# Kernel optimization log

Hardware: AMD Instinct MI355X
Metric: run time of the kernel (lower is better)

The kernel has to match this reference:

```python
import jax, jax.numpy as jnp
import numpy as np

D = 256
B, S, N = 4, 512, 4


def setup_inputs() -> dict:
    key = jax.random.key(0)
    ks = jax.random.split(key, 24)
    d, dq = D, D // 4
    std = 0.02
    inp = {
        'x':   jax.random.normal(ks[0], (B, S, N, d), jnp.float32),
        'Wq':  jax.random.normal(ks[1], (d, d), jnp.float32) * std,
        'Wk':  jax.random.normal(ks[2], (d, d), jnp.float32) * std,
        'Wv':  jax.random.normal(ks[3], (d, d), jnp.float32) * std,
        'Wg1': jax.random.normal(ks[4], (d, d), jnp.float32) * std,
        'bg1': jnp.zeros((d,), jnp.float32),
        'Wg2': jax.random.normal(ks[5], (d, d), jnp.float32) * std,
        'bg2': jnp.zeros((d,), jnp.float32),
        'We1': jax.random.normal(ks[6], (d, dq), jnp.float32) * std,
        'be1': jnp.zeros((dq,), jnp.float32),
        'We2': jax.random.normal(ks[7], (dq, 1), jnp.float32) * std,
        'be2': jnp.zeros((1,), jnp.float32),
        'Wa1': jax.random.normal(ks[8], (d, dq), jnp.float32) * std,
        'ba1': jnp.zeros((dq,), jnp.float32),
        'Wa2': jax.random.normal(ks[9], (dq, 1), jnp.float32) * std,
        'ba2': jnp.zeros((1,), jnp.float32),
        'Wo':  jax.random.normal(ks[10], (d, d), jnp.float32) * std,
        'bo':  jnp.zeros((d,), jnp.float32),
        'gamma': jnp.ones((d,), jnp.float32),
        'beta':  jnp.zeros((d,), jnp.float32),
    }
    return inp


def reference(x, Wq, Wk, Wv, Wg1, bg1, Wg2, bg2, We1, be1, We2, be2,
              Wa1, ba1, Wa2, ba2, Wo, bo, gamma, beta):
    b, s, n, f = x.shape
    xf = x.reshape(b * n, s, f)  # matches torch .view on contiguous x
    residual = xf

    q = xf @ Wq                                    # [bn, s, d]
    k = xf @ Wk
    v = xf @ Wv
    v_hat = jax.nn.silu(v @ Wg1 + bg1) @ Wg2 + bg2  # value_generator
    eta = jax.nn.sigmoid(jax.nn.silu(xf @ We1 + be1) @ We2 + be2) * 0.1 + 0.01   # [bn, s, 1]
    alpha = jax.nn.sigmoid(jax.nn.silu(xf @ Wa1 + ba1) @ Wa2 + ba2) * 0.5 + 0.5  # [bn, s, 1]

    # F.normalize(k, dim=-1): eps = 1e-12
    kn = k / jnp.maximum(jnp.linalg.norm(k, axis=-1, keepdims=True), 1e-12)

    M0 = jnp.zeros((b * n, f, f), x.dtype)

    def step(M, inp):
        q_t, k_t, v_t, e_t, a_t = inp  # [bn,d],[bn,d],[bn,d],[bn,1],[bn,1]
        out_t = jnp.einsum('bij,bj->bi', M, q_t)
        Mk = jnp.einsum('bij,bj->bi', M, k_t)
        e = e_t[:, :, None]  # [bn,1,1]
        a = a_t[:, :, None]
        # delta rule: M <- a*M - e*(Mk k^T) + e*(v k^T)
        M_new = a * M + e * ((v_t - Mk)[:, :, None] * k_t[:, None, :])
        return M_new, out_t

    seq = (jnp.swapaxes(q, 0, 1), jnp.swapaxes(kn, 0, 1), jnp.swapaxes(v_hat, 0, 1),
           jnp.swapaxes(eta, 0, 1), jnp.swapaxes(alpha, 0, 1))
    M, outs = jax.lax.scan(step, M0, seq)
    out = jnp.swapaxes(outs, 0, 1)  # [bn, s, d]

    y = out @ Wo + bo + residual  # dropout is identity in eval/reference
    mu = jnp.mean(y, axis=-1, keepdims=True)
    var = jnp.var(y, axis=-1, keepdims=True)
    y = (y - mu) / jnp.sqrt(var + 1e-5) * gamma + beta
    return y.reshape(b, s, n, f), M
```

## Files before the change

kernel.cpp:

```cpp
#include <hip/hip_runtime.h>

#define F_ 256
#define S_ 512
#define NH_ 16
#define CCH 32
#define NCH (S_/CCH)
#define KSTR 264
#define KTSTR 36
#define TSTR 40
#define PSTR 17

typedef __attribute__((ext_vector_type(8))) short short8_t;
typedef __attribute__((ext_vector_type(4))) float f32x4;

__device__ __forceinline__ float sigmoid_f(float x) { return 1.0f / (1.0f + __expf(-x)); }

__device__ __forceinline__ ushort f2bf(float x) {
  uint u = __float_as_uint(x);
  u += 0x7FFFu + ((u >> 16) & 1u);
  return (ushort)(u >> 16);
}
__device__ __forceinline__ float bf2f(ushort u) {
  return __uint_as_float((uint)u << 16);
}

template<int CTRL>
__device__ __forceinline__ float dpp_add(float x) {
  int y = __builtin_amdgcn_update_dpp(0, __float_as_int(x), CTRL, 0xf, 0xf, true);
  return x + __int_as_float(y);
}
__device__ __forceinline__ float red8(float x) {
  x = dpp_add<0xB1>(x);
  x = dpp_add<0x4E>(x);
  x = dpp_add<0x141>(x);
  return x;
}

__global__ __launch_bounds__(256) void wconv_k(
    const float* __restrict__ Wq, const float* __restrict__ Wk,
    const float* __restrict__ Wv, const float* __restrict__ Wg1,
    const float* __restrict__ Wg2, const float* __restrict__ Wo,
    const float* __restrict__ We1, const float* __restrict__ Wa1,
    const float* __restrict__ be1, const float* __restrict__ ba1,
    const float* __restrict__ x,
    ushort* __restrict__ Wt, float* __restrict__ beas,
    ushort* __restrict__ xb)
{
  const int blk = blockIdx.x, tid = threadIdx.x;
  if (blk >= 105) {
    const size_t base = (size_t)(blk - 105) * 16384;
    #pragma unroll
    for (int p = 0; p < 16; ++p) {
      const size_t o = base + (size_t)(((p << 8) + tid) << 2);
      const float4 v = *(const float4*)&x[o];
      ushort4 h4;
      h4.x = f2bf(v.x); h4.y = f2bf(v.y); h4.z = f2bf(v.z); h4.w = f2bf(v.w);
      *(ushort4*)&xb[o] = h4;
    }
    return;
  }
  if (blk == 104) {
    if (tid < 64) beas[tid] = be1[tid];
    else if (tid < 128) beas[tid] = ba1[tid - 64];
    return;
  }
  __shared__ float tile[64][65];
  const float* src; int N, k0, n0; size_t dstbase;
  if (blk < 96) {
    const int w = blk >> 4, tl = blk & 15;
    const float* ws_[6] = {Wq, Wk, Wv, Wg1, Wg2, Wo};
    const size_t dstb[6] = {0, 65536, 131072, 229376, 294912, 360448};
    src = ws_[w]; N = 256;
    k0 = (tl >> 2) * 64; n0 = (tl & 3) * 64;
    dstbase = dstb[w];
  } else {
    const int w = (blk - 96) >> 2, tl = (blk - 96) & 3;
    src = w ? Wa1 : We1; N = 64;
    k0 = tl * 64; n0 = 0;
    dstbase = w ? 212992 : 196608;
  }
  #pragma unroll
  for (int p = 0; p < 4; ++p) {
    const int idx = (p << 8) + tid;
    const int r = idx >> 4, c4 = (idx & 15) << 2;
    if (c4 < N) {
      const float4 v = *(const float4*)&src[(size_t)(k0 + r) * N + n0 + c4];
      tile[r][c4 + 0] = v.x; tile[r][c4 + 1] = v.y;
      tile[r][c4 + 2] = v.z; tile[r][c4 + 3] = v.w;
    }
  }
  __syncthreads();
  #pragma unroll
  for (int p = 0; p < 4; ++p) {
    const int idx = (p << 8) + tid;
    const int nl = idx >> 4, kc = (idx & 15) << 2;
    if (nl < ((blk < 96) ? 64 : 64) && (n0 + nl) < ((blk < 96) ? 256 : 64)) {
      ushort4 o;
      o.x = f2bf(tile[kc + 0][nl]); o.y = f2bf(tile[kc + 1][nl]);
      o.z = f2bf(tile[kc + 2][nl]); o.w = f2bf(tile[kc + 3][nl]);
      *(ushort4*)&Wt[dstbase + (size_t)(n0 + nl) * 256 + k0 + kc] = o;
    }
  }
}

__global__ __launch_bounds__(256) void qkve_k(
    const ushort* __restrict__ A, const ushort* __restrict__ Wt,
    const float* __restrict__ beas,
    ushort* __restrict__ qb, float* __restrict__ kf,
    ushort* __restrict__ vb, float* __restrict__ sesa)
{
  __shared__ ushort As[2][64 * 72];
  __shared__ ushort Ws[2][64 * 72];
  const int tid = threadIdx.x;
  const int wv = tid >> 6, l = tid & 63;
  const int ln = l & 15, hi = l >> 4, hi4 = hi << 2, hi8 = hi << 3;
  const int wr = wv >> 1, wc = wv & 1;
  const int row0 = blockIdx.y * 64, col0 = blockIdx.x * 64;
  const int r_ = tid >> 3, c8_ = (tid & 7) << 3;

  short8_t pA[2], pB[2];
  auto loadT = [&](int k0) {
    pA[0] = *(const short8_t*)&A[(size_t)(row0 + r_) * 256 + k0 + c8_];
    pA[1] = *(const short8_t*)&A[(size_t)(row0 + 32 + r_) * 256 + k0 + c8_];
    pB[0] = *(const short8_t*)&Wt[(size_t)(col0 + r_) * 256 + k0 + c8_];
    pB[1] = *(const short8_t*)&Wt[(size_t)(col0 + 32 + r_) * 256 + k0 + c8_];
  };
  auto commitT = [&](int b) {
    *(short8_t*)&As[b][r_ * 72 + c8_] = pA[0];
    *(short8_t*)&As[b][(32 + r_) * 72 + c8_] = pA[1];
    *(short8_t*)&Ws[b][r_ * 72 + c8_] = pB[0];
    *(short8_t*)&Ws[b][(32 + r_) * 72 + c8_] = pB[1];
  };

  f32x4 acc[2][2];
  #pragma unroll
  for (int i = 0; i < 2; ++i)
    #pragma unroll
    for (int j = 0; j < 2; ++j)
      #pragma unroll
      for (int r = 0; r < 4; ++r) acc[i][j][r] = 0.f;

  loadT(0); commitT(0); __syncthreads();
  #pragma unroll
  for (int t = 0; t < 4; ++t) {
    const int b = t & 1;
    if (t < 3) loadT((t + 1) << 6);
    #pragma unroll
    for (int kk = 0; kk < 2; ++kk) {
      short8_t a0 = *(const short8_t*)&As[b][(wr * 32 + ln) * 72 + kk * 32 + hi8];
      short8_t a1 = *(const short8_t*)&As[b][(wr * 32 + 16 + ln) * 72 + kk * 32 + hi8];
      short8_t b0 = *(const short8_t*)&Ws[b][(wc * 32 + ln) * 72 + kk * 32 + hi8];
      short8_t b1 = *(const short8_t*)&Ws[b][(wc * 32 + 16 + ln) * 72 + kk * 32 + hi8];
      acc[0][0] = __builtin_amdgcn_mfma_f32_16x16x32_bf16(a0, b0, acc[0][0], 0, 0, 0);
      acc[0][1] = __builtin_amdgcn_mfma_f32_16x16x32_bf16(a0, b1, acc[0][1], 0, 0, 0);
      acc[1][0] = __builtin_amdgcn_mfma_f32_16x16x32_bf16(a1, b0, acc[1][0], 0, 0, 0);
      acc[1][1] = __builtin_amdgcn_mfma_f32_16x16x32_bf16(a1, b1, acc[1][1], 0, 0, 0);
    }
    if (t < 3) commitT(b ^ 1);
    __syncthreads();
  }

  #pragma unroll
  for (int mi = 0; mi < 2; ++mi)
    #pragma unroll
    for (int ni = 0; ni < 2; ++ni) {
      const int col = col0 + wc * 32 + ni * 16 + ln;
      #pragma unroll
      for (int r = 0; r < 4; ++r) {
        const int row = row0 + wr * 32 + mi * 16 + hi4 + r;
        float vx = acc[mi][ni][r];
        if (col0 < 256)      qb[(size_t)row * 256 + col] = f2bf(vx);
        else if (col0 < 512) kf[(size_t)row * 256 + (col - 256)] = vx;
        else if (col0 < 768) vb[(size_t)row * 256 + (col - 512)] = f2bf(vx);
        else {
          const int cc = col - 768;
          vx += beas[cc];
          vx *= sigmoid_f(vx);
          sesa[(size_t)row * 128 + cc] = vx;
        }
      }
    }
}

__global__ __launch_bounds__(256) void gemm_bf16_k(
    const ushort* __restrict__ A, const ushort* __restrict__ Wt,
    const float* __restrict__ bias, float* __restrict__ Cf,
    ushort* __restrict__ Cb, int act)
{
  __shared__ ushort As[2][64 * 72];
  __shared__ ushort Ws[2][64 * 72];
  const int tid = threadIdx.x;
  const int wv = tid >> 6, l = tid & 63;
  const int ln = l & 15, hi = l >> 4, hi4 = hi << 2, hi8 = hi << 3;
  const int wr = wv >> 1, wc = wv & 1;
  const int row0 = blockIdx.y * 64, col0 = blockIdx.x * 64;
  const int r_ = tid >> 3, c8_ = (tid & 7) << 3;

  short8_t pA[2], pB[2];
  auto loadT = [&](int k0) {
    pA[0] = *(const short8_t*)&A[(size_t)(row0 + r_) * 256 + k0 + c8_];
    pA[1] = *(const short8_t*)&A[(size_t)(row0 + 32 + r_) * 256 + k0 + c8_];
    pB[0] = *(const short8_t*)&Wt[(size_t)(col0 + r_) * 256 + k0 + c8_];
    pB[1] = *(const short8_t*)&Wt[(size_t)(col0 + 32 + r_) * 256 + k0 + c8_];
  };
  auto commitT = [&](int b) {
    *(short8_t*)&As[b][r_ * 72 + c8_] = pA[0];
    *(short8_t*)&As[b][(32 + r_) * 72 + c8_] = pA[1];
    *(short8_t*)&Ws[b][r_ * 72 + c8_] = pB[0];
    *(short8_t*)&Ws[b][(32 + r_) * 72 + c8_] = pB[1];
  };

  f32x4 acc[2][2];
  #pragma unroll
  for (int i = 0; i < 2; ++i)
    #pragma unroll
    for (int j = 0; j < 2; ++j)
      #pragma unroll
      for (int r = 0; r < 4; ++r) acc[i][j][r] = 0.f;

  loadT(0); commitT(0); __syncthreads();
  #pragma unroll
  for (int t = 0; t < 4; ++t) {
    const int b = t & 1;
    if (t < 3) loadT((t + 1) << 6);
    #pragma unroll
    for (int kk = 0; kk < 2; ++kk) {
      short8_t a0 = *(const short8_t*)&As[b][(wr * 32 + ln) * 72 + kk * 32 + hi8];
      short8_t a1 = *(const short8_t*)&As[b][(wr * 32 + 16 + ln) * 72 + kk * 32 + hi8];
      short8_t b0 = *(const short8_t*)&Ws[b][(wc * 32 + ln) * 72 + kk * 32 + hi8];
      short8_t b1 = *(const short8_t*)&Ws[b][(wc * 32 + 16 + ln) * 72 + kk * 32 + hi8];
      acc[0][0] = __builtin_amdgcn_mfma_f32_16x16x32_bf16(a0, b0, acc[0][0], 0, 0, 0);
      acc[0][1] = __builtin_amdgcn_mfma_f32_16x16x32_bf16(a0, b1, acc[0][1], 0, 0, 0);
      acc[1][0] = __builtin_amdgcn_mfma_f32_16x16x32_bf16(a1, b0, acc[1][0], 0, 0, 0);
      acc[1][1] = __builtin_amdgcn_mfma_f32_16x16x32_bf16(a1, b1, acc[1][1], 0, 0, 0);
    }
    if (t < 3) commitT(b ^ 1);
    __syncthreads();
  }

  #pragma unroll
  for (int mi = 0; mi < 2; ++mi)
    #pragma unroll
    for (int ni = 0; ni < 2; ++ni) {
      const int col = col0 + wc * 32 + ni * 16 + ln;
      const float bval = bias ? bias[col] : 0.f;
      #pragma unroll
      for (int r = 0; r < 4; ++r) {
        const int row = row0 + wr * 32 + mi * 16 + hi4 + r;
        float vx = acc[mi][ni][r] + bval;
        if (act == 1) vx = vx * sigmoid_f(vx);
        if (Cf) Cf[(size_t)row * 256 + col] = vx;
        if (Cb) Cb[(size_t)row * 256 + col] = f2bf(vx);
      }
    }
}

__global__ __launch_bounds__(256) void knea_k(
    const float* __restrict__ kf, ushort* __restrict__ kb,
    const float* __restrict__ sesa,
    const float* __restrict__ We2, const float* __restrict__ be2,
    const float* __restrict__ Wa2, const float* __restrict__ ba2,
    float* __restrict__ eta, float* __restrict__ alpha)
{
  const int lane = threadIdx.x & 63;
  const size_t row = ((size_t)blockIdx.x << 2) + (threadIdx.x >> 6);
  {
    const size_t off = row * F_ + ((size_t)lane << 2);
    float4 v = *(const float4*)&kf[off];
    float ss = v.x * v.x + v.y * v.y + v.z * v.z + v.w * v.w;
    #pragma unroll
    for (int m = 1; m < 64; m <<= 1) ss += __shfl_xor(ss, m, 64);
    const float sc = 1.0f / fmaxf(sqrtf(ss), 1e-12f);
    ushort4 o;
    o.x = f2bf(v.x * sc); o.y = f2bf(v.y * sc);
    o.z = f2bf(v.z * sc); o.w = f2bf(v.w * sc);
    *(ushort4*)&kb[off] = o;
  }
  {
    float pe = sesa[row * 128 + lane] * We2[lane];
    float pa = sesa[row * 128 + 64 + lane] * Wa2[lane];
    #pragma unroll
    for (int m = 1; m < 64; m <<= 1) {
      pe += __shfl_xor(pe, m, 64);
      pa += __shfl_xor(pa, m, 64);
    }
    if (lane == 0) {
      eta[row]   = sigmoid_f(pe + be2[0]) * 0.1f + 0.01f;
      alpha[row] = sigmoid_f(pa + ba2[0]) * 0.5f + 0.5f;
    }
  }
}

__global__ __launch_bounds__(256) void ln_k(
    const float* __restrict__ t, const float* __restrict__ x,
    const float* __restrict__ gamma, const float* __restrict__ beta,
    float* __restrict__ y)
{
  const int lane = threadIdx.x & 63;
  const size_t row = ((size_t)blockIdx.x << 2) + (threadIdx.x >> 6);
  const size_t off = row * F_ + ((size_t)lane << 2);
  const float4 tv = *(const float4*)&t[off];
  const float4 xv = *(const float4*)&x[off];
  float4 v = make_float4(tv.x + xv.x, tv.y + xv.y, tv.z + xv.z, tv.w + xv.w);
  float sm = v.x + v.y + v.z + v.w;
  float sq = v.x * v.x + v.y * v.y + v.z * v.z + v.w * v.w;
  #pragma unroll
  for (int m = 1; m < 64; m <<= 1) {
    sm += __shfl_xor(sm, m, 64);
    sq += __shfl_xor(sq, m, 64);
  }
  const float mu  = sm * (1.0f / 256.0f);
  const float var = sq * (1.0f / 256.0f) - mu * mu;
  const float rstd = rsqrtf(var + 1e-5f);
  const float4 g = *(const float4*)&gamma[(size_t)lane << 2];
  const float4 b = *(const float4*)&beta[(size_t)lane << 2];
  float4 o;
  o.x = (v.x - mu) * rstd * g.x + b.x;
  o.y = (v.y - mu) * rstd * g.y + b.y;
  o.z = (v.z - mu) * rstd * g.z + b.z;
  o.w = (v.w - mu) * rstd * g.w + b.w;
  *(float4*)&y[off] = o;
}

__global__ __launch_bounds__(256) void prep_k(
    const ushort* __restrict__ kb, const ushort* __restrict__ qb,
    const float* __restrict__ eta, const float* __restrict__ alpha,
    ushort* __restrict__ Tg, ushort* __restrict__ Gqg, float* __restrict__ Sg,
    ushort* __restrict__ Ktg)
{
  __shared__ ushort K_lds[CCH * KSTR];
  __shared__ ushort Q_lds[CCH * KSTR];
  __shared__ float  G_lds[CCH * CCH];
  __shared__ float  ea[2 * CCH];
  __shared__ float  scal[100];

  const int tid = threadIdx.x;
  const int ch = blockIdx.x, h = blockIdx.y;
  const int t0 = ch * CCH;
  const int l = tid & 63, wv = tid >> 6;
  const int ln = l & 15, hi = l >> 4;
  const int hi8 = hi * 8, hi4 = hi * 4;

  const ushort* kg = kb + (size_t)(h * S_ + t0) * F_;
  const ushort* qg = qb + (size_t)(h * S_ + t0) * F_;
  #pragma unroll
  for (int w = 0; w < 4; ++w) {
    int o = w * 256 + tid; int t = o >> 5, c8 = (o & 31) << 3;
    *(short8_t*)&K_lds[t * KSTR + c8] = *(const short8_t*)&kg[(size_t)t * F_ + c8];
    *(short8_t*)&Q_lds[t * KSTR + c8] = *(const short8_t*)&qg[(size_t)t * F_ + c8];
  }
  if (tid < CCH)            ea[tid] = eta[(size_t)h * S_ + t0 + tid];
  else if (tid < 2 * CCH)   ea[tid] = alpha[(size_t)h * S_ + t0 + tid - CCH];
  __syncthreads();

  {
    const int tt = tid & 31, cl = tid >> 5;
    for (int cp = 0; cp < 32; ++cp) {
      const int c = cp * 8 + cl;
      Ktg[((size_t)h * F_ + c) * S_ + t0 + tt] = K_lds[tt * KSTR + c];
    }
  }

  {
    const int tI = wv >> 1, tJ = wv & 1;
    f32x4 accG = {0.f, 0.f, 0.f, 0.f};
    f32x4 accQ = {0.f, 0.f, 0.f, 0.f};
    #pragma unroll
    for (int ko = 0; ko < 8; ++ko) {
      const int cb = ko * 32 + hi8;
      short8_t bfr = *(const short8_t*)&K_lds[(tJ * 16 + ln) * KSTR + cb];
      short8_t aK  = *(const short8_t*)&K_lds[(tI * 16 + ln) * KSTR + cb];
      short8_t aQ  = *(const short8_t*)&Q_lds[(tI * 16 + ln) * KSTR + cb];
      accG = __builtin_amdgcn_mfma_f32_16x16x32_bf16(aK, bfr, accG, 0, 0, 0);
      accQ = __builtin_amdgcn_mfma_f32_16x16x32_bf16(aQ, bfr, accQ, 0, 0, 0);
    }
    ushort* Gqo = Gqg + (size_t)(h * NCH + ch) * (CCH * CCH);
    #pragma unroll
    for (int r = 0; r < 4; ++r) {
      const int t = tI * 16 + hi4 + r, s = tJ * 16 + ln;
      G_lds[t * CCH + s] = accG[r];
      Gqo[t * CCH + s] = (s < t) ? f2bf(accQ[r]) : (ushort)0;
    }
  }
  if (tid == 0) {
    float gp = 1.f;
    for (int t = 0; t < CCH; ++t) {
      const float a = ea[CCH + t], e = ea[t];
      const float gm = gp * a;
      scal[t]           = e / a;
      scal[CCH + t]     = e / gm;
      scal[2 * CCH + t] = gp;
      gp = gm;
    }
    scal[3 * CCH] = gp;
  }
  __syncthreads();

  {
    const int j = tid >> 3, g = tid & 7;
    float x0 = 0.f, x1 = 0.f, x2 = 0.f, x3 = 0.f;
    ushort* To = Tg + (size_t)(h * NCH + ch) * (CCH * CCH);
    #pragma unroll
    for (int t = 0; t < CCH; ++t) {
      float p = 0.f;
      const f32x4 gr = *(const f32x4*)&G_lds[t * CCH + 4 * g];
      if (4 * g + 0 < t) p += gr[0] * x0;
      if (4 * g + 1 < t) p += gr[1] * x1;
      if (4 * g + 2 < t) p += gr[2] * x2;
      if (4 * g + 3 < t) p += gr[3] * x3;
      const float tot = red8(p);
      const float xt = ((t == j) ? 1.f : 0.f) - scal[t] * tot;
      if (g == (t >> 2)) {
        if ((t & 3) == 0) x0 = xt; else if ((t & 3) == 1) x1 = xt;
        else if ((t & 3) == 2) x2 = xt; else x3 = xt;
      }
      if (g == 0) To[t * CCH + j] = f2bf(xt);
    }
  }
  if (tid < 97) Sg[(size_t)(h * NCH + ch) * 128 + tid] = scal[tid];
}

__global__ __launch_bounds__(256, 1) void scan_chunk_k(
    const ushort* __restrict__ kb, const ushort* __restrict__ qb,
    const ushort* __restrict__ vhb, const ushort* __restrict__ Ktg,
    const ushort* __restrict__ Tg, const ushort* __restrict__ Gqg,
    const float* __restrict__ Sg,
    ushort* __restrict__ outb, float* __restrict__ Mout)
{
  __shared__ ushort K_lds[CCH * KSTR];
  __shared__ ushort Q_lds[CCH * KSTR];
  __shared__ ushort Kt_lds[2][F_ * KTSTR];
  __shared__ ushort M_lds[2][16 * KSTR];
  __shared__ ushort T_lds[CCH * TSTR];
  __shared__ ushort Gq_lds[2][CCH * TSTR];
  __shared__ ushort Wt_lds[16 * TSTR];
  __shared__ ushort R_lds[16 * TSTR];
  __shared__ float  KMp[4 * CCH * PSTR];
  __shared__ float  QM_lds[CCH * PSTR];
  __shared__ ushort V_lds[CCH * 16];
  __shared__ float  scal[2][104];

  const int tid = threadIdx.x;
  const int flat = blockIdx.x;
  const int h = (flat & 7) + ((flat >> 7) << 3);
  const int slice = (flat >> 3) & 15;
  const int r0 = slice * 16;
  const int wv = tid >> 6, l = tid & 63;
  const int ln = l & 15, hi = l >> 4, hi4 = hi << 2, hi8 = hi << 3;

  for (int u = tid; u < 16 * KSTR / 8; u += 256) {
    short8_t z = {0, 0, 0, 0, 0, 0, 0, 0};
    *(short8_t*)&M_lds[0][u * 8] = z;
  }
  f32x4 Mf[4];
  #pragma unroll
  for (int q = 0; q < 4; ++q)
    #pragma unroll
    for (int r = 0; r < 4; ++r) Mf[q][r] = 0.f;

  const ushort* kgh = kb + (size_t)h * S_ * F_;
  const ushort* qgh = qb + (size_t)h * S_ * F_;
  const ushort* kth = Ktg + (size_t)h * F_ * S_;

  short8_t pK[4], pQ[4], pKt[4], pTG;
  ushort pV[2]; float pS = 0.f;

  auto loadchunk = [&](int ch) {
    const int t0 = ch * CCH;
    #pragma unroll
    for (int r = 0; r < 4; ++r) {
      const int idx = (r << 8) + tid;
      const int t = idx >> 5, c8 = (idx & 31) << 3;
      pK[r] = *(const short8_t*)&kgh[(size_t)(t0 + t) * F_ + c8];
      pQ[r] = *(const short8_t*)&qgh[(size_t)(t0 + t) * F_ + c8];
    }
    #pragma unroll
    for (int r = 0; r < 4; ++r) {
      const int idx = (r << 8) + tid;
      const int c = idx >> 2, t8 = (idx & 3) << 3;
      pKt[r] = *(const short8_t*)&kth[(size_t)c * S_ + t0 + t8];
    }
    #pragma unroll
    for (int u = 0; u < 2; ++u) {
      const int e = (u << 8) + tid, t = e >> 4, i = e & 15;
      pV[u] = vhb[(size_t)(h * S_ + t0 + t) * F_ + r0 + i];
    }
    {
      const ushort* Ti = Tg  + (size_t)(h * NCH + ch) * (CCH * CCH);
      const ushort* Gi = Gqg + (size_t)(h * NCH + ch) * (CCH * CCH);
      if (tid < 128) {
        const int t = tid >> 2, c8 = (tid & 3) << 3;
        pTG = *(const short8_t*)&Ti[t * CCH + c8];
      } else {
        const int t = (tid - 128) >> 2, c8 = ((tid - 128) & 3) << 3;
        pTG = *(const short8_t*)&Gi[t * CCH + c8];
      }
    }
    if (tid < 97) pS = Sg[(size_t)(h * NCH + ch) * 128 + tid];
  };

  auto commit = [&](int b) {
    #pragma unroll
    for (int r = 0; r < 4; ++r) {
      const int idx = (r << 8) + tid;
      const int t = idx >> 5, c8 = (idx & 31) << 3;
      *(short8_t*)&K_lds[t * KSTR + c8] = pK[r];
      *(short8_t*)&Q_lds[t * KSTR + c8] = pQ[r];
    }
    #pragma unroll
    for (int r = 0; r < 4; ++r) {
      const int idx = (r << 8) + tid;
      const int c = idx >> 2, t8 = (idx & 3) << 3;
      *(short8_t*)&Kt_lds[b][c * KTSTR + t8] = pKt[r];
    }
    #pragma unroll
    for (int u = 0; u < 2; ++u) V_lds[(u << 8) + tid] = pV[u];
    if (tid < 128) {
      const int t = tid >> 2, c8 = (tid & 3) << 3;
      *(short8_t*)&T_lds[t * TSTR + c8] = pTG;
    } else {
      const int t = (tid - 128) >> 2, c8 = ((tid - 128) & 3) << 3;
      *(short8_t*)&Gq_lds[b][t * TSTR + c8] = pTG;
    }
    if (tid < 97) scal[b][tid] = pS;
  };

  loadchunk(0);
  commit(0);
  __syncthreads();
  int cb = 0;

  for (int ch = 0; ch < NCH; ++ch) {
    const int t0 = ch * CCH;
    const int nb = cb ^ 1;
    if (ch + 1 < NCH) loadchunk(ch + 1);

    {
      const int j0 = wv * 64;
      f32x4 a0v = {0.f, 0.f, 0.f, 0.f};
      f32x4 a1v = {0.f, 0.f, 0.f, 0.f};
      #pragma unroll
      for (int ks = 0; ks < 2; ++ks) {
        const int jc = j0 + ks * 32 + hi8;
        short8_t bm = *(const short8_t*)&M_lds[cb][ln * KSTR + jc];
        short8_t a0 = *(const short8_t*)&K_lds[ln * KSTR + jc];
        short8_t a1 = *(const short8_t*)&K_lds[(16 + ln) * KSTR + jc];
        a0v = __builtin_amdgcn_mfma_f32_16x16x32_bf16(a0, bm, a0v, 0, 0, 0);
        a1v = __builtin_amdgcn_mfma_f32_16x16x32_bf16(a1, bm, a1v, 0, 0, 0);
      }
      #pragma unroll
      for (int r = 0; r < 4; ++r) {
        KMp[wv * (CCH * PSTR) + (hi4 + r) * PSTR + ln] = a0v[r];
        KMp[wv * (CCH * PSTR) + (16 + hi4 + r) * PSTR + ln] = a1v[r];
      }
    }
    __syncthreads();

    if (wv == 0) {
      const int i = l & 15, tg = l >> 4;
      short8_t rv;
      #pragma unroll
      for (int u = 0; u < 8; ++u) {
        const int t = tg * 8 + u;
        const float s = KMp[t * PSTR + i]
                      + KMp[CCH * PSTR + t * PSTR + i]
                      + KMp[2 * CCH * PSTR + t * PSTR + i]
                      + KMp[3 * CCH * PSTR + t * PSTR + i];
        const float rhs = scal[cb][CCH + t] * bf2f(V_lds[t * 16 + i])
                        - scal[cb][t] * s;
        rv[u] = (short)f2bf(rhs);
      }
      *(short8_t*)&R_lds[i * TSTR + tg * 8] = rv;
      #pragma unroll
      for (int I = 0; I < 2; ++I) {
        short8_t a = *(const short8_t*)&T_lds[(I * 16 + ln) * TSTR + hi8];
        short8_t b = *(const short8_t*)&R_lds[ln * TSTR + hi8];
        f32x4 z = {0.f, 0.f, 0.f, 0.f};
        f32x4 d = __builtin_amdgcn_mfma_f32_16x16x32_bf16(a, b, z, 0, 0, 0);
        ushort4 wo;
        wo.x = f2bf(d[0]); wo.y = f2bf(d[1]); wo.z = f2bf(d[2]); wo.w = f2bf(d[3]);
        *(ushort4*)&Wt_lds[ln * TSTR + I * 16 + hi4] = wo;
      }
    } else if (wv >= 2) {
      const int I = wv - 2;
      f32x4 acc = {0.f, 0.f, 0.f, 0.f};
      #pragma unroll
      for (int ko = 0; ko < 8; ++ko) {
        short8_t a = *(const short8_t*)&Q_lds[(I * 16 + ln) * KSTR + ko * 32 + hi8];
        short8_t b = *(const short8_t*)&M_lds[cb][ln * KSTR + ko * 32 + hi8];
        acc = __builtin_amdgcn_mfma_f32_16x16x32_bf16(a, b, acc, 0, 0, 0);
      }
      #pragma unroll
      for (int r = 0; r < 4; ++r)
        QM_lds[(I * 16 + hi4 + r) * PSTR + ln] = acc[r];
    }
    __syncthreads();

    {
      const float gC = scal[cb][3 * CCH];
      short8_t aw = *(const short8_t*)&Wt_lds[ln * TSTR + hi8];
      #pragma unroll
      for (int qq = 0; qq < 4; ++qq) {
        const int jt = wv * 4 + qq;
        short8_t bk = *(const short8_t*)&Kt_lds[cb][(jt * 16 + ln) * KTSTR + hi8];
        f32x4 d = __builtin_amdgcn_mfma_f32_16x16x32_bf16(aw, bk, Mf[qq], 0, 0, 0);
        #pragma unroll
        for (int r = 0; r < 4; ++r) {
          const float nv = gC * d[r];
          Mf[qq][r] = nv;
          M_lds[nb][(hi4 + r) * KSTR + jt * 16 + ln] = f2bf(nv);
        }
      }
    }
    if (wv < 2) {
      const int I = wv;
      short8_t a = *(const short8_t*)&Gq_lds[cb][(I * 16 + ln) * TSTR + hi8];
      short8_t b = *(const short8_t*)&Wt_lds[ln * TSTR + hi8];
      f32x4 z = {0.f, 0.f, 0.f, 0.f};
      f32x4 d = __builtin_amdgcn_mfma_f32_16x16x32_bf16(a, b, z, 0, 0, 0);
      #pragma unroll
      for (int r = 0; r < 4; ++r) {
        const int t = I * 16 + hi4 + r;
        const float ov = scal[cb][2 * CCH + t] * (QM_lds[t * PSTR + ln] + d[r]);
        outb[(size_t)(h * S_ + t0 + t) * F_ + r0 + ln] = f2bf(ov);
      }
    }
    if (ch + 1 < NCH) commit(nb);
    __syncthreads();
    cb = nb;
  }

  #pragma unroll
  for (int qq = 0; qq < 4; ++qq) {
    const int jt = wv * 4 + qq;
    #pragma unroll
    for (int r = 0; r < 4; ++r)
      Mout[((size_t)h * F_ + r0 + hi4 + r) * F_ + jt * 16 + ln] = Mf[qq][r];
  }
}

extern "C" void kernel_launch(void* const* d_in, const int* in_sizes, int n_in,
                              void* d_out, int out_size, void* d_ws, size_t ws_size,
                              hipStream_t stream)
{
  const float* x    = (const float*)d_in[0];
  const float* Wq   = (const float*)d_in[1];
  const float* Wk   = (const float*)d_in[2];
  const float* Wv   = (const float*)d_in[3];
  const float* Wg1  = (const float*)d_in[4];
  const float* bg1  = (const float*)d_in[5];
  const float* Wg2  = (const float*)d_in[6];
  const float* bg2  = (const float*)d_in[7];
  const float* We1  = (const float*)d_in[8];
  const float* be1  = (const float*)d_in[9];
  const float* We2  = (const float*)d_in[10];
  const float* be2  = (const float*)d_in[11];
  const float* Wa1  = (const float*)d_in[12];
  const float* ba1  = (const float*)d_in[13];
  const float* Wa2  = (const float*)d_in[14];
  const float* ba2  = (const float*)d_in[15];
  const float* Wo   = (const float*)d_in[16];
  const float* bo   = (const float*)d_in[17];
  const float* gamma= (const float*)d_in[18];
  const float* beta = (const float*)d_in[19];

  const int Mrows = NH_ * S_;
  const size_t MM = 1048576;
  const size_t NTF = 2 * MM;

  float* ws = (float*)d_ws;
  ushort* xb   = (ushort*)(ws + 0 * MM);
  ushort* outb = (ushort*)(ws + 0 * MM);
  ushort* qb   = (ushort*)(ws + 1 * MM);
  ushort* kb   = (ushort*)(ws + 2 * MM);
  float*  kf   = ws + 3 * MM;
  ushort* t1b  = (ushort*)(ws + 3 * MM);
  ushort* vhb  = (ushort*)(ws + 4 * MM);
  ushort* vb   = (ushort*)(ws + 5 * MM);
  float*  sesa = ws + 6 * MM;
  float*  ytmp = ws + 5 * MM;
  float*  eta  = ws + 7 * MM;
  float*  alpha= eta + Mrows;
  ushort* Tg   = (ushort*)(ws + 7 * MM + 16384);
  ushort* Gqg  = Tg + 262144;
  float*  Sg   = ws + 7 * MM + 16384 + 131072 + 131072;
  ushort* Ktg  = (ushort*)(Sg + 32768);
  ushort* Wt   = Ktg + 2097152;
  float*  beas = (float*)(Wt + 425984);

  dim3 blk(256);

  wconv_k<<<233, blk, 0, stream>>>(Wq, Wk, Wv, Wg1, Wg2, Wo, We1, Wa1,
                                   be1, ba1, x, Wt, beas, xb);

  qkve_k<<<dim3(14, 128), blk, 0, stream>>>(xb, Wt, beas, qb, kf, vb, sesa);

  knea_k<<<Mrows / 4, blk, 0, stream>>>(kf, kb, sesa, We2, be2, Wa2, ba2, eta, alpha);

  gemm_bf16_k<<<dim3(4, 128), blk, 0, stream>>>(vb,  Wt + 229376, bg1, nullptr, t1b, 1);
  gemm_bf16_k<<<dim3(4, 128), blk, 0, stream>>>(t1b, Wt + 294912, bg2, nullptr, vhb, 0);

  prep_k<<<dim3(NCH, NH_), blk, 0, stream>>>(kb, qb, eta, alpha, Tg, Gqg, Sg, Ktg);

  float* yout = (float*)d_out;
  float* Mfin = yout + NTF;
  scan_chunk_k<<<256, blk, 0, stream>>>(kb, qb, vhb, Ktg, Tg, Gqg, Sg, outb, Mfin);

  gemm_bf16_k<<<dim3(4, 128), blk, 0, stream>>>(outb, Wt + 360448, bo, ytmp, nullptr, 0);
  ln_k<<<Mrows / 4, blk, 0, stream>>>(ytmp, x, gamma, beta, yout);
}
```

Baseline: 101.2 us.

## Restructure chunked scan: two row-slices per 512-thread block, MFMA operands from registers

The chunked delta-rule scan kernel now runs 512-thread blocks, each handling two 16-row slices of the state matrix. K, Q, K-transpose and the T/Gq operands are loaded straight into registers in MFMA fragment layout, so the LDS staging buffers, the commit pass and most LDS traffic go away. Work is also reassigned across waves: K·M and Q·M are split over four waves, which halves the KMp reduction. In exchange, each block is larger, only 128 blocks are launched, register pressure rises, and global loads for K-transpose now sit on the critical path within each chunk.

```diff
diff --git a/kernel.cpp b/kernel.cpp
--- a/kernel.cpp
+++ b/kernel.cpp
@@ -6,9 +6,7 @@
 #define CCH 32
 #define NCH (S_/CCH)
 #define KSTR 264
-#define KTSTR 36
 #define TSTR 40
-#define PSTR 17
 
 typedef __attribute__((ext_vector_type(8))) short short8_t;
 typedef __attribute__((ext_vector_type(4))) float f32x4;
@@ -94,7 +92,7 @@
   for (int p = 0; p < 4; ++p) {
     const int idx = (p << 8) + tid;
     const int nl = idx >> 4, kc = (idx & 15) << 2;
-    if (nl < ((blk < 96) ? 64 : 64) && (n0 + nl) < ((blk < 96) ? 256 : 64)) {
+    if ((n0 + nl) < ((blk < 96) ? 256 : 64)) {
       ushort4 o;
       o.x = f2bf(tile[kc + 0][nl]); o.y = f2bf(tile[kc + 1][nl]);
       o.z = f2bf(tile[kc + 2][nl]); o.w = f2bf(tile[kc + 3][nl]);
@@ -420,36 +418,40 @@
   if (tid < 97) Sg[(size_t)(h * NCH + ch) * 128 + tid] = scal[tid];
 }
 
-__global__ __launch_bounds__(256, 1) void scan_chunk_k(
+__global__ __launch_bounds__(512, 1) void scan_chunk_k(
     const ushort* __restrict__ kb, const ushort* __restrict__ qb,
     const ushort* __restrict__ vhb, const ushort* __restrict__ Ktg,
     const ushort* __restrict__ Tg, const ushort* __restrict__ Gqg,
     const float* __restrict__ Sg,
     ushort* __restrict__ outb, float* __restrict__ Mout)
 {
-  __shared__ ushort K_lds[CCH * KSTR];
-  __shared__ ushort Q_lds[CCH * KSTR];
-  __shared__ ushort Kt_lds[2][F_ * KTSTR];
   __shared__ ushort M_lds[2][16 * KSTR];
-  __shared__ ushort T_lds[CCH * TSTR];
-  __shared__ ushort Gq_lds[2][CCH * TSTR];
-  __shared__ ushort Wt_lds[16 * TSTR];
-  __shared__ ushort R_lds[16 * TSTR];
-  __shared__ float  KMp[4 * CCH * PSTR];
-  __shared__ float  QM_lds[CCH * PSTR];
-  __shared__ ushort V_lds[CCH * 16];
-  __shared__ float  scal[2][104];
+  __shared__ float  KMp[2][2 * CCH * 17];
+  __shared__ float  QM_lds[2][CCH * 17];
+  __shared__ ushort R_lds[2][16 * TSTR];
+  __shared__ ushort Wt_lds[2][16 * TSTR];
+  __shared__ ushort V_lds[2][CCH * 16];
+  __shared__ float  scal_lds[100];
 
   const int tid = threadIdx.x;
+  const int wave = tid >> 6;
+  const int cn = wave >> 2;
+  const int wv4 = wave & 3;
+  const int l = tid & 63;
+  const int ln = l & 15, hi = l >> 4, hi4 = hi << 2, hi8 = hi << 3;
   const int flat = blockIdx.x;
-  const int h = (flat & 7) + ((flat >> 7) << 3);
-  const int slice = (flat >> 3) & 15;
+  const int h = (flat & 7) + (((flat >> 3) & 1) << 3);
+  const int sp = flat >> 4;
+  const int slice = sp * 2 + cn;
   const int r0 = slice * 16;
-  const int wv = tid >> 6, l = tid & 63;
-  const int ln = l & 15, hi = l >> 4, hi4 = hi << 2, hi8 = hi << 3;
-
-  for (int u = tid; u < 16 * KSTR / 8; u += 256) {
-    short8_t z = {0, 0, 0, 0, 0, 0, 0, 0};
+
+  const ushort* kgh = kb  + (size_t)h * S_ * F_;
+  const ushort* qgh = qb  + (size_t)h * S_ * F_;
+  const ushort* kth = Ktg + (size_t)h * F_ * S_;
+  const ushort* vgh = vhb + (size_t)h * S_ * F_;
+
+  for (int u = tid; u < 2 * 16 * KSTR / 8; u += 512) {
+    short8_t z = {0,0,0,0,0,0,0,0};
     *(short8_t*)&M_lds[0][u * 8] = z;
   }
   f32x4 Mf[4];
@@ -458,181 +460,145 @@
     #pragma unroll
     for (int r = 0; r < 4; ++r) Mf[q][r] = 0.f;
 
-  const ushort* kgh = kb + (size_t)h * S_ * F_;
-  const ushort* qgh = qb + (size_t)h * S_ * F_;
-  const ushort* kth = Ktg + (size_t)h * F_ * S_;
-
-  short8_t pK[4], pQ[4], pKt[4], pTG;
-  ushort pV[2]; float pS = 0.f;
-
-  auto loadchunk = [&](int ch) {
+  short8_t pP1[8];
+  float pS = 0.f;
+  auto loadP1 = [&](int ch) {
     const int t0 = ch * CCH;
-    #pragma unroll
-    for (int r = 0; r < 4; ++r) {
-      const int idx = (r << 8) + tid;
-      const int t = idx >> 5, c8 = (idx & 31) << 3;
-      pK[r] = *(const short8_t*)&kgh[(size_t)(t0 + t) * F_ + c8];
-      pQ[r] = *(const short8_t*)&qgh[(size_t)(t0 + t) * F_ + c8];
-    }
-    #pragma unroll
-    for (int r = 0; r < 4; ++r) {
-      const int idx = (r << 8) + tid;
-      const int c = idx >> 2, t8 = (idx & 3) << 3;
-      pKt[r] = *(const short8_t*)&kth[(size_t)c * S_ + t0 + t8];
-    }
-    #pragma unroll
-    for (int u = 0; u < 2; ++u) {
-      const int e = (u << 8) + tid, t = e >> 4, i = e & 15;
-      pV[u] = vhb[(size_t)(h * S_ + t0 + t) * F_ + r0 + i];
-    }
-    {
-      const ushort* Ti = Tg  + (size_t)(h * NCH + ch) * (CCH * CCH);
-      const ushort* Gi = Gqg + (size_t)(h * NCH + ch) * (CCH * CCH);
-      if (tid < 128) {
-        const int t = tid >> 2, c8 = (tid & 3) << 3;
-        pTG = *(const short8_t*)&Ti[t * CCH + c8];
-      } else {
-        const int t = (tid - 128) >> 2, c8 = ((tid - 128) & 3) << 3;
-        pTG = *(const short8_t*)&Gi[t * CCH + c8];
-      }
-    }
+    if (wv4 < 2) {
+      #pragma unroll
+      for (int tt = 0; tt < 2; ++tt)
+        #pragma unroll
+        for (int ks = 0; ks < 4; ++ks)
+          pP1[tt * 4 + ks] = *(const short8_t*)
+            &kgh[(size_t)(t0 + tt * 16 + ln) * 256 + wv4 * 128 + ks * 32 + hi8];
+    } else {
+      const int t16 = (wv4 - 2) * 16;
+      #pragma unroll
+      for (int ko = 0; ko < 8; ++ko)
+        pP1[ko] = *(const short8_t*)
+          &qgh[(size_t)(t0 + t16 + ln) * 256 + ko * 32 + hi8];
+    }
+  };
+  auto loadS = [&](int ch) {
     if (tid < 97) pS = Sg[(size_t)(h * NCH + ch) * 128 + tid];
   };
 
-  auto commit = [&](int b) {
-    #pragma unroll
-    for (int r = 0; r < 4; ++r) {
-      const int idx = (r << 8) + tid;
-      const int t = idx >> 5, c8 = (idx & 31) << 3;
-      *(short8_t*)&K_lds[t * KSTR + c8] = pK[r];
-      *(short8_t*)&Q_lds[t * KSTR + c8] = pQ[r];
-    }
-    #pragma unroll
-    for (int r = 0; r < 4; ++r) {
-      const int idx = (r << 8) + tid;
-      const int c = idx >> 2, t8 = (idx & 3) << 3;
-      *(short8_t*)&Kt_lds[b][c * KTSTR + t8] = pKt[r];
-    }
-    #pragma unroll
-    for (int u = 0; u < 2; ++u) V_lds[(u << 8) + tid] = pV[u];
-    if (tid < 128) {
-      const int t = tid >> 2, c8 = (tid & 3) << 3;
-      *(short8_t*)&T_lds[t * TSTR + c8] = pTG;
-    } else {
-      const int t = (tid - 128) >> 2, c8 = ((tid - 128) & 3) << 3;
-      *(short8_t*)&Gq_lds[b][t * TSTR + c8] = pTG;
-    }
-    if (tid < 97) scal[b][tid] = pS;
-  };
-
-  loadchunk(0);
-  commit(0);
+  loadP1(0); loadS(0);
   __syncthreads();
-  int cb = 0;
 
   for (int ch = 0; ch < NCH; ++ch) {
     const int t0 = ch * CCH;
-    const int nb = cb ^ 1;
-    if (ch + 1 < NCH) loadchunk(ch + 1);
-
-    {
-      const int j0 = wv * 64;
-      f32x4 a0v = {0.f, 0.f, 0.f, 0.f};
-      f32x4 a1v = {0.f, 0.f, 0.f, 0.f};
-      #pragma unroll
-      for (int ks = 0; ks < 2; ++ks) {
-        const int jc = j0 + ks * 32 + hi8;
-        short8_t bm = *(const short8_t*)&M_lds[cb][ln * KSTR + jc];
-        short8_t a0 = *(const short8_t*)&K_lds[ln * KSTR + jc];
-        short8_t a1 = *(const short8_t*)&K_lds[(16 + ln) * KSTR + jc];
-        a0v = __builtin_amdgcn_mfma_f32_16x16x32_bf16(a0, bm, a0v, 0, 0, 0);
-        a1v = __builtin_amdgcn_mfma_f32_16x16x32_bf16(a1, bm, a1v, 0, 0, 0);
-      }
-      #pragma unroll
-      for (int r = 0; r < 4; ++r) {
-        KMp[wv * (CCH * PSTR) + (hi4 + r) * PSTR + ln] = a0v[r];
-        KMp[wv * (CCH * PSTR) + (16 + hi4 + r) * PSTR + ln] = a1v[r];
-      }
+
+    if (tid < 97) scal_lds[tid] = pS;
+
+    short8_t pKt[4];
+    #pragma unroll
+    for (int qq = 0; qq < 4; ++qq) {
+      const int jt = wv4 * 4 + qq;
+      pKt[qq] = *(const short8_t*)&kth[(size_t)(jt * 16 + ln) * S_ + t0 + hi8];
+    }
+    short8_t pAux0 = {0,0,0,0,0,0,0,0}, pAux1 = {0,0,0,0,0,0,0,0};
+    if (wv4 == 0) {
+      const size_t tb = (size_t)(h * NCH + ch) * (CCH * CCH);
+      pAux0 = *(const short8_t*)&Tg[tb + (size_t)(0 * 16 + ln) * CCH + hi8];
+      pAux1 = *(const short8_t*)&Tg[tb + (size_t)(1 * 16 + ln) * CCH + hi8];
+    } else if (wv4 >= 2) {
+      const int I = wv4 - 2;
+      pAux0 = *(const short8_t*)
+        &Gqg[(size_t)(h * NCH + ch) * (CCH * CCH) + (size_t)(I * 16 + ln) * CCH + hi8];
+    }
+    if (wv4 == 1 && l < 32) {
+      short8_t v0 = *(const short8_t*)&vgh[(size_t)(t0 + l) * 256 + r0];
+      short8_t v1 = *(const short8_t*)&vgh[(size_t)(t0 + l) * 256 + r0 + 8];
+      *(short8_t*)&V_lds[cn][l * 16] = v0;
+      *(short8_t*)&V_lds[cn][l * 16 + 8] = v1;
+    }
+
+    if (wv4 < 2) {
+      #pragma unroll
+      for (int tt = 0; tt < 2; ++tt) {
+        f32x4 acc = {0.f, 0.f, 0.f, 0.f};
+        #pragma unroll
+        for (int ks = 0; ks < 4; ++ks) {
+          const int jc = wv4 * 128 + ks * 32 + hi8;
+          short8_t bm = *(const short8_t*)&M_lds[cn][ln * KSTR + jc];
+          acc = __builtin_amdgcn_mfma_f32_16x16x32_bf16(pP1[tt * 4 + ks], bm, acc, 0, 0, 0);
+        }
+        #pragma unroll
+        for (int r = 0; r < 4; ++r)
+          KMp[cn][wv4 * (CCH * 17) + (tt * 16 + hi4 + r) * 17 + ln] = acc[r];
+      }
+    } else {
+      const int t16 = (wv4 - 2) * 16;
+      f32x4 acc = {0.f, 0.f, 0.f, 0.f};
+      #pragma unroll
+      for (int ko = 0; ko < 8; ++ko) {
+        short8_t bm = *(const short8_t*)&M_lds[cn][ln * KSTR + ko * 32 + hi8];
+        acc = __builtin_amdgcn_mfma_f32_16x16x32_bf16(pP1[ko], bm, acc, 0, 0, 0);
+      }
+      #pragma unroll
+      for (int r = 0; r < 4; ++r)
+        QM_lds[cn][(t16 + hi4 + r) * 17 + ln] = acc[r];
     }
     __syncthreads();
 
-    if (wv == 0) {
-      const int i = l & 15, tg = l >> 4;
+    if (ch + 1 < NCH) { loadP1(ch + 1); loadS(ch + 1); }
+    if (wv4 == 0) {
       short8_t rv;
       #pragma unroll
       for (int u = 0; u < 8; ++u) {
-        const int t = tg * 8 + u;
-        const float s = KMp[t * PSTR + i]
-                      + KMp[CCH * PSTR + t * PSTR + i]
-                      + KMp[2 * CCH * PSTR + t * PSTR + i]
-                      + KMp[3 * CCH * PSTR + t * PSTR + i];
-        const float rhs = scal[cb][CCH + t] * bf2f(V_lds[t * 16 + i])
-                        - scal[cb][t] * s;
+        const int t = hi * 8 + u;
+        const float s = KMp[cn][t * 17 + ln] + KMp[cn][CCH * 17 + t * 17 + ln];
+        const float rhs = scal_lds[CCH + t] * bf2f(V_lds[cn][t * 16 + ln])
+                        - scal_lds[t] * s;
         rv[u] = (short)f2bf(rhs);
       }
-      *(short8_t*)&R_lds[i * TSTR + tg * 8] = rv;
+      *(short8_t*)&R_lds[cn][ln * TSTR + hi8] = rv;
       #pragma unroll
       for (int I = 0; I < 2; ++I) {
-        short8_t a = *(const short8_t*)&T_lds[(I * 16 + ln) * TSTR + hi8];
-        short8_t b = *(const short8_t*)&R_lds[ln * TSTR + hi8];
+        short8_t a = (I == 0) ? pAux0 : pAux1;
+        short8_t b = *(const short8_t*)&R_lds[cn][ln * TSTR + hi8];
         f32x4 z = {0.f, 0.f, 0.f, 0.f};
         f32x4 d = __builtin_amdgcn_mfma_f32_16x16x32_bf16(a, b, z, 0, 0, 0);
         ushort4 wo;
         wo.x = f2bf(d[0]); wo.y = f2bf(d[1]); wo.z = f2bf(d[2]); wo.w = f2bf(d[3]);
-        *(ushort4*)&Wt_lds[ln * TSTR + I * 16 + hi4] = wo;
-      }
-    } else if (wv >= 2) {
-      const int I = wv - 2;
-      f32x4 acc = {0.f, 0.f, 0.f, 0.f};
-      #pragma unroll
-      for (int ko = 0; ko < 8; ++ko) {
-        short8_t a = *(const short8_t*)&Q_lds[(I * 16 + ln) * KSTR + ko * 32 + hi8];
-        short8_t b = *(const short8_t*)&M_lds[cb][ln * KSTR + ko * 32 + hi8];
-        acc = __builtin_amdgcn_mfma_f32_16x16x32_bf16(a, b, acc, 0, 0, 0);
-      }
-      #pragma unroll
-      for (int r = 0; r < 4; ++r)
-        QM_lds[(I * 16 + hi4 + r) * PSTR + ln] = acc[r];
+        *(ushort4*)&Wt_lds[cn][ln * TSTR + I * 16 + hi4] = wo;
+      }
     }
     __syncthreads();
 
     {
-      const float gC = scal[cb][3 * CCH];
-      short8_t aw = *(const short8_t*)&Wt_lds[ln * TSTR + hi8];
+      const float gC = scal_lds[3 * CCH];
+      short8_t aw = *(const short8_t*)&Wt_lds[cn][ln * TSTR + hi8];
       #pragma unroll
       for (int qq = 0; qq < 4; ++qq) {
-        const int jt = wv * 4 + qq;
-        short8_t bk = *(const short8_t*)&Kt_lds[cb][(jt * 16 + ln) * KTSTR + hi8];
-        f32x4 d = __builtin_amdgcn_mfma_f32_16x16x32_bf16(aw, bk, Mf[qq], 0, 0, 0);
+        const int jt = wv4 * 4 + qq;
+        f32x4 d = __builtin_amdgcn_mfma_f32_16x16x32_bf16(aw, pKt[qq], Mf[qq], 0, 0, 0);
         #pragma unroll
         for (int r = 0; r < 4; ++r) {
-          const float nv = gC * d[r];
-          Mf[qq][r] = nv;
-          M_lds[nb][(hi4 + r) * KSTR + jt * 16 + ln] = f2bf(nv);
+          Mf[qq][r] = gC * d[r];
+          M_lds[cn][(hi4 + r) * KSTR + jt * 16 + ln] = f2bf(Mf[qq][r]);
         }
       }
     }
-    if (wv < 2) {
-      const int I = wv;
-      short8_t a = *(const short8_t*)&Gq_lds[cb][(I * 16 + ln) * TSTR + hi8];
-      short8_t b = *(const short8_t*)&Wt_lds[ln * TSTR + hi8];
+    if (wv4 >= 2) {
+      const int I = wv4 - 2;
+      short8_t b = *(const short8_t*)&Wt_lds[cn][ln * TSTR + hi8];
       f32x4 z = {0.f, 0.f, 0.f, 0.f};
-      f32x4 d = __builtin_amdgcn_mfma_f32_16x16x32_bf16(a, b, z, 0, 0, 0);
+      f32x4 d = __builtin_amdgcn_mfma_f32_16x16x32_bf16(pAux0, b, z, 0, 0, 0);
       #pragma unroll
       for (int r = 0; r < 4; ++r) {
         const int t = I * 16 + hi4 + r;
-        const float ov = scal[cb][2 * CCH + t] * (QM_lds[t * PSTR + ln] + d[r]);
+        const float ov = scal_lds[2 * CCH + t] * (QM_lds[cn][t * 17 + ln] + d[r]);
         outb[(size_t)(h * S_ + t0 + t) * F_ + r0 + ln] = f2bf(ov);
       }
     }
-    if (ch + 1 < NCH) commit(nb);
     __syncthreads();
-    cb = nb;
   }
 
   #pragma unroll
   for (int qq = 0; qq < 4; ++qq) {
-    const int jt = wv * 4 + qq;
+    const int jt = wv4 * 4 + qq;
     #pragma unroll
     for (int r = 0; r < 4; ++r)
       Mout[((size_t)h * F_ + r0 + hi4 + r) * F_ + jt * 16 + ln] = Mf[qq][r];
@@ -704,7 +670,7 @@
 
   float* yout = (float*)d_out;
   float* Mfin = yout + NTF;
-  scan_chunk_k<<<256, blk, 0, stream>>>(kb, qb, vhb, Ktg, Tg, Gqg, Sg, outb, Mfin);
+  scan_chunk_k<<<128, dim3(512), 0, stream>>>(kb, qb, vhb, Ktg, Tg, Gqg, Sg, outb, Mfin);
 
   gemm_bf16_k<<<dim3(4, 128), blk, 0, stream>>>(outb, Wt + 360448, bo, ytmp, nullptr, 0);
   ln_k<<<Mrows / 4, blk, 0, stream>>>(ytmp, x, gamma, beta, yout);
```

Measured after the change: 123.7 us. +22.2%, slower.
